# Kernel tuning notes

Hardware: AMD Instinct MI355X
Metric: run time of the kernel (lower is better)

## Reference

```python
import jax, jax.numpy as jnp
import numpy as np

N_HEADS = 32
N_KV = 8
GROUPS = 4
D_HEAD = 64
ROPE_BASE = 10000.0


def _rope_tables(seq_len):
    # inv_freq over even dims, emb = [freqs, freqs] along last axis (torch cat([outer]*2))
    inv_freq = 1.0 / (ROPE_BASE ** (jnp.arange(0, D_HEAD, 2, dtype=jnp.float32) / D_HEAD))
    t = jnp.arange(seq_len, dtype=jnp.float32)
    freqs = jnp.outer(t, inv_freq)                      # [S, D_HEAD/2]
    emb = jnp.concatenate([freqs, freqs], axis=-1)      # [S, D_HEAD]
    return jnp.cos(emb), jnp.sin(emb)


def _rotate_half(x):
    h = x.shape[-1] // 2
    return jnp.concatenate([-x[..., h:], x[..., :h]], axis=-1)


def setup_inputs() -> dict:
    key = jax.random.key(0)
    ks = jax.random.split(key, 5)
    B, S, D = 4, 2048, 2048
    s = 0.02
    return {
        "x": jax.random.normal(ks[0], (B, S, D), dtype=jnp.float32),
        "Wq": jax.random.normal(ks[1], (D, D), dtype=jnp.float32) * s,
        "Wk": jax.random.normal(ks[2], (N_KV * D_HEAD, D), dtype=jnp.float32) * s,
        "Wv": jax.random.normal(ks[3], (N_KV * D_HEAD, D), dtype=jnp.float32) * s,
        "Wo": jax.random.normal(ks[4], (D, D), dtype=jnp.float32) * s,
        "temperature": jnp.float32(1.0),
    }


def reference(x, Wq, Wk, Wv, Wo, temperature):
    B, S, D = x.shape
    # QKV projections (torch Linear: x @ W.T)
    Q = jnp.einsum('bsd,ed->bse', x, Wq).reshape(B, S, N_HEADS, D_HEAD).transpose(0, 2, 1, 3)
    K = jnp.einsum('bsd,ed->bse', x, Wk).reshape(B, S, N_KV, D_HEAD).transpose(0, 2, 1, 3)
    V = jnp.einsum('bsd,ed->bse', x, Wv).reshape(B, S, N_KV, D_HEAD).transpose(0, 2, 1, 3)

    # RoPE (offset=0, no past_kv)
    cos, sin = _rope_tables(S)          # [S, D_HEAD]
    cos = cos[None, None]
    sin = sin[None, None]
    Q = Q * cos + _rotate_half(Q) * sin
    K = K * cos + _rotate_half(K) * sin

    kv_cache = (K, V)  # pre-expansion cache, as in original

    # GQA expand: each kv head repeated GROUPS times along head axis
    Ke = jnp.repeat(K, GROUPS, axis=1)  # [B, N_HEADS, S, D_HEAD]
    Ve = jnp.repeat(V, GROUPS, axis=1)

    # scale uses .item() in torch -> constant w.r.t. autograd
    scale = (D_HEAD ** -0.5) / jnp.maximum(jnp.abs(temperature), 1e-6)
    scale = jax.lax.stop_gradient(scale)

    scores = jnp.einsum('bhqd,bhkd->bhqk', Q, Ke) * scale
    causal = jnp.tril(jnp.ones((S, S), dtype=bool))
    scores = jnp.where(causal[None, None], scores, jnp.finfo(scores.dtype).min)
    attn = jax.nn.softmax(scores, axis=-1)
    out = jnp.einsum('bhqk,bhkd->bhqd', attn, Ve)       # [B, H, S, D_HEAD]

    out = out.transpose(0, 2, 1, 3).reshape(B, S, D)
    y = jnp.einsum('bsd,ed->bse', out, Wo)
    return (y, kv_cache[0], kv_cache[1])
```

## Files before the change

kernel.cpp:

```cpp
#include <hip/hip_runtime.h>

#define S_LEN  2048
#define DMODEL 2048
#define NH     32
#define NKV    8
#define DH     64

typedef _Float16 h8   __attribute__((ext_vector_type(8)));
typedef _Float16 h4   __attribute__((ext_vector_type(4)));
typedef float    f32x4 __attribute__((ext_vector_type(4)));

__device__ __forceinline__ void load_lds16(const _Float16* g, _Float16* l) {
  typedef const __attribute__((address_space(1))) unsigned int* gp_t;
  typedef __attribute__((address_space(3))) unsigned int* lp_t;
  __builtin_amdgcn_global_load_lds((gp_t)g, (lp_t)l, 16, 0, 0);
}

#define N8_X  2097152
#define N8_WQ 524288
#define N8_WK 131072
#define N8_WV 131072
#define N8_WO 524288
#define N8_ALL (N8_X + N8_WQ + N8_WK + N8_WV + N8_WO)
__global__ void cvt_all(const float* __restrict__ x, const float* __restrict__ wq,
                        const float* __restrict__ wk, const float* __restrict__ wv,
                        const float* __restrict__ wo, _Float16* __restrict__ dst) {
  int stride = gridDim.x * blockDim.x;
  for (int i = blockIdx.x * blockDim.x + threadIdx.x; i < N8_ALL; i += stride) {
    const float* s;
    int off;
    if (i < N8_X) { s = x; off = i; }
    else if (i < N8_X + N8_WQ) { s = wq; off = i - N8_X; }
    else if (i < N8_X + N8_WQ + N8_WK) { s = wk; off = i - (N8_X + N8_WQ); }
    else if (i < N8_X + N8_WQ + N8_WK + N8_WV) { s = wv; off = i - (N8_X + N8_WQ + N8_WK); }
    else { s = wo; off = i - (N8_X + N8_WQ + N8_WK + N8_WV); }
    float4 a = ((const float4*)s)[2 * off];
    float4 b = ((const float4*)s)[2 * off + 1];
    h8 v = {(_Float16)a.x, (_Float16)a.y, (_Float16)a.z, (_Float16)a.w,
            (_Float16)b.x, (_Float16)b.y, (_Float16)b.z, (_Float16)b.w};
    ((h8*)dst)[i] = v;
  }
}

__global__ void rope_table_k(float2* __restrict__ tab) {
  int i = blockIdx.x * blockDim.x + threadIdx.x;
  int s = i >> 5, d = i & 31;
  float invf = (float)exp2(-(double)d * 0.4152410118609203);
  float angf = (float)s * invf;
  double a = (double)angf;
  const double twopi = 6.283185307179586476925287;
  a -= floor(a / twopi) * twopi;
  tab[i] = make_float2((float)cos(a), (float)sin(a));
}

template <int MODE>
__global__ __launch_bounds__(256) void gemm128(
    const _Float16* __restrict__ A, const _Float16* __restrict__ Bm,
    _Float16* __restrict__ qH, _Float16* __restrict__ kH, float* __restrict__ kF,
    _Float16* __restrict__ vH, float* __restrict__ vF, float* __restrict__ yF,
    const float2* __restrict__ rtab, const float* __restrict__ tptr) {
  __shared__ __align__(16) _Float16 lA[128 * 32];
  __shared__ __align__(16) _Float16 lB[128 * 32];
  const int Kd = 2048;
  int t = threadIdx.x;
  int w = t >> 6, lane = t & 63;
  int n0 = blockIdx.x * 128, m0 = blockIdx.y * 128;
  int wr = w >> 1, wc = w & 1;
  int lq = lane & 15, hi = lane >> 4;

  const _Float16* gA = A + (size_t)(m0 + w * 32 + (lane >> 2)) * Kd + (lane & 3) * 8;
  const _Float16* gB = Bm + (size_t)(n0 + w * 32 + (lane >> 2)) * Kd + (lane & 3) * 8;
  _Float16* dA0 = &lA[(w * 32) * 32];
  _Float16* dA1 = &lA[(w * 32 + 16) * 32];
  _Float16* dB0 = &lB[(w * 32) * 32];
  _Float16* dB1 = &lB[(w * 32 + 16) * 32];

  f32x4 z4 = {0.f, 0.f, 0.f, 0.f};
  f32x4 acc[4][4];
#pragma unroll
  for (int i = 0; i < 4; i++)
#pragma unroll
    for (int j = 0; j < 4; j++) acc[i][j] = z4;

  for (int k0 = 0; k0 < Kd; k0 += 32) {
    __syncthreads();
    load_lds16(gA + k0, dA0);
    load_lds16(gA + (size_t)16 * Kd + k0, dA1);
    load_lds16(gB + k0, dB0);
    load_lds16(gB + (size_t)16 * Kd + k0, dB1);
    __syncthreads();
    h8 af[4], bf[4];
#pragma unroll
    for (int i = 0; i < 4; i++)
      af[i] = *(const h8*)&lA[(wr * 64 + i * 16 + lq) * 32 + hi * 8];
#pragma unroll
    for (int j = 0; j < 4; j++)
      bf[j] = *(const h8*)&lB[(wc * 64 + j * 16 + lq) * 32 + hi * 8];
#pragma unroll
    for (int i = 0; i < 4; i++)
#pragma unroll
      for (int j = 0; j < 4; j++)
        acc[i][j] = __builtin_amdgcn_mfma_f32_16x16x32_f16(af[i], bf[j], acc[i][j], 0, 0, 0);
  }

  if (MODE == 3) {
#pragma unroll
    for (int ci = 0; ci < 4; ci++) {
      int col = n0 + wc * 64 + ci * 16 + lq;
#pragma unroll
      for (int ri = 0; ri < 4; ri++)
#pragma unroll
        for (int r = 0; r < 4; r++) {
          int m = m0 + wr * 64 + ri * 16 + hi * 4 + r;
          yF[(size_t)m * DMODEL + col] = acc[ri][ci][r];
        }
    }
  } else {
    int base64 = n0 + wc * 64;
    if (base64 < 2048) {
      float qsc = 0.125f / fmaxf(fabsf(tptr[0]), 1e-6f) * 1.4426950408889634f;
      int head = base64 >> 6;
#pragma unroll
      for (int ci = 0; ci < 2; ci++) {
        int dlo = ci * 16 + lq;
#pragma unroll
        for (int ri = 0; ri < 4; ri++)
#pragma unroll
          for (int r = 0; r < 4; r++) {
            int m = m0 + wr * 64 + ri * 16 + hi * 4 + r;
            int b = m >> 11, s = m & 2047;
            float2 cs = rtab[s * 32 + dlo];
            float lo = acc[ri][ci][r], hv = acc[ri][ci + 2][r];
            float olo = (lo * cs.x - hv * cs.y) * qsc;
            float ohi = (hv * cs.x + lo * cs.y) * qsc;
            size_t base = ((size_t)(b * NH + head) * S_LEN + s) * DH;
            qH[base + dlo] = (_Float16)olo;
            qH[base + dlo + 32] = (_Float16)ohi;
          }
      }
    } else if (base64 < 2560) {
      int head = (base64 - 2048) >> 6;
#pragma unroll
      for (int ci = 0; ci < 2; ci++) {
        int dlo = ci * 16 + lq;
#pragma unroll
        for (int ri = 0; ri < 4; ri++)
#pragma unroll
          for (int r = 0; r < 4; r++) {
            int m = m0 + wr * 64 + ri * 16 + hi * 4 + r;
            int b = m >> 11, s = m & 2047;
            float2 cs = rtab[s * 32 + dlo];
            float lo = acc[ri][ci][r], hv = acc[ri][ci + 2][r];
            float olo = lo * cs.x - hv * cs.y;
            float ohi = hv * cs.x + lo * cs.y;
            size_t bb = ((size_t)(b * NKV + head) * S_LEN + s) * DH;
            kH[bb + dlo] = (_Float16)olo;
            kH[bb + dlo + 32] = (_Float16)ohi;
            kF[bb + dlo] = olo;
            kF[bb + dlo + 32] = ohi;
          }
      }
    } else {
      int head = (base64 - 2560) >> 6;
#pragma unroll
      for (int ci = 0; ci < 4; ci++) {
        int d = ci * 16 + lq;
#pragma unroll
        for (int ri = 0; ri < 4; ri++)
#pragma unroll
          for (int r = 0; r < 4; r++) {
            int m = m0 + wr * 64 + ri * 16 + hi * 4 + r;
            int b = m >> 11, s = m & 2047;
            float v = acc[ri][ci][r];
            vH[((size_t)(b * NKV + head) * DH + d) * S_LEN + s] = (_Float16)v;
            vF[((size_t)(b * NKV + head) * S_LEN + s) * DH + d] = v;
          }
      }
    }
  }
}

__global__ __launch_bounds__(256, 3) void attn_fwd(
    const _Float16* __restrict__ Q, const _Float16* __restrict__ K,
    const _Float16* __restrict__ Vt, _Float16* __restrict__ AO) {
  __shared__ __align__(16) _Float16 lP[4][32 * 72];
  __shared__ __align__(16) _Float16 lV[2][64 * 64];
  int t = threadIdx.x, w = t >> 6, lane = t & 63;
  int lq = lane & 15, hi = lane >> 4;

  int bh = blockIdx.x * 16 + (blockIdx.y & 15);
  int qb = 15 - (blockIdx.y >> 4);
  int b = bh >> 5, h = bh & 31, g = h >> 2;

  const _Float16* Qp = Q + ((size_t)(b * NH + h) * S_LEN) * DH;
  const _Float16* Kp = K + ((size_t)(b * NKV + g) * S_LEN) * DH;
  const _Float16* Vp = Vt + ((size_t)(b * NKV + g) * DH) * S_LEN;

  f32x4 z4 = {0.f, 0.f, 0.f, 0.f};
  int q0 = qb * 128 + w * 32;

  size_t so0 = (size_t)(w * 16 + (lane >> 3)) * S_LEN + (size_t)(((lane & 7) ^ (lane >> 3)) * 8);
  size_t so1 = so0 + (size_t)8 * S_LEN;

  h8 qf[2][2];
#pragma unroll
  for (int cf = 0; cf < 2; cf++)
#pragma unroll
    for (int dc = 0; dc < 2; dc++)
      qf[cf][dc] = *(const h8*)&Qp[(size_t)(q0 + lq + 16 * cf) * DH + dc * 32 + hi * 8];

  f32x4 ot[4][2];
#pragma unroll
  for (int rf = 0; rf < 4; rf++)
#pragma unroll
    for (int cf = 0; cf < 2; cf++) ot[rf][cf] = z4;
  float mrun[2] = {-3e38f, -3e38f};
  float lrun[2] = {0.f, 0.f};

  int NT = 2 * qb + 2;

  load_lds16(Vp + so0, &lV[0][(w * 16) * 64]);
  load_lds16(Vp + so1, &lV[0][(w * 16 + 8) * 64]);
  h8 kf[2][4];
#pragma unroll
  for (int dc = 0; dc < 2; dc++)
#pragma unroll
    for (int rf = 0; rf < 4; rf++)
      kf[dc][rf] = *(const h8*)&Kp[(size_t)(rf * 16 + lq) * DH + dc * 32 + hi * 8];

  for (int tk = 0; tk < NT; tk++) {
    int kv0 = tk * 64;

    f32x4 sc[4][2];
#pragma unroll
    for (int rf = 0; rf < 4; rf++)
#pragma unroll
      for (int cf = 0; cf < 2; cf++) sc[rf][cf] = z4;
#pragma unroll
    for (int dc = 0; dc < 2; dc++)
#pragma unroll
      for (int rf = 0; rf < 4; rf++)
#pragma unroll
        for (int cf = 0; cf < 2; cf++)
          sc[rf][cf] = __builtin_amdgcn_mfma_f32_16x16x32_f16(kf[dc][rf], qf[cf][dc], sc[rf][cf], 0, 0, 0);

    {
      int kvn = kv0 + 64;
#pragma unroll
      for (int dc = 0; dc < 2; dc++)
#pragma unroll
        for (int rf = 0; rf < 4; rf++)
          kf[dc][rf] = *(const h8*)&Kp[(size_t)(kvn + rf * 16 + lq) * DH + dc * 32 + hi * 8];
    }

    if (kv0 + 63 > q0) {
#pragma unroll
      for (int rf = 0; rf < 4; rf++)
#pragma unroll
        for (int cf = 0; cf < 2; cf++)
#pragma unroll
          for (int r = 0; r < 4; r++) {
            int kv = kv0 + rf * 16 + hi * 4 + r;
            int q = q0 + lq + 16 * cf;
            if (kv > q) sc[rf][cf][r] = -1e30f;
          }
    }

    float mt[2];
#pragma unroll
    for (int cf = 0; cf < 2; cf++) {
      float m2 = -3e38f;
#pragma unroll
      for (int rf = 0; rf < 4; rf++)
#pragma unroll
        for (int r = 0; r < 4; r++) m2 = fmaxf(m2, sc[rf][cf][r]);
      m2 = fmaxf(m2, __shfl_xor(m2, 16));
      m2 = fmaxf(m2, __shfl_xor(m2, 32));
      mt[cf] = m2;
    }

    bool need = !__all((mt[0] - mrun[0] <= 8.f) && (mt[1] - mrun[1] <= 8.f));
    if (need) {
#pragma unroll
      for (int cf = 0; cf < 2; cf++) {
        float mnew = fmaxf(mrun[cf], mt[cf]);
        float al = __builtin_amdgcn_exp2f(mrun[cf] - mnew);
        mrun[cf] = mnew;
        lrun[cf] *= al;
#pragma unroll
        for (int rf = 0; rf < 4; rf++)
#pragma unroll
          for (int r = 0; r < 4; r++) ot[rf][cf][r] *= al;
      }
    }

    float ls[2] = {0.f, 0.f};
#pragma unroll
    for (int rf = 0; rf < 4; rf++)
#pragma unroll
      for (int cf = 0; cf < 2; cf++)
#pragma unroll
        for (int r = 0; r < 4; r++) {
          float p = __builtin_amdgcn_exp2f(sc[rf][cf][r] - mrun[cf]);
          sc[rf][cf][r] = p;
          ls[cf] += p;
        }
#pragma unroll
    for (int cf = 0; cf < 2; cf++) {
      float s2 = ls[cf];
      s2 += __shfl_xor(s2, 16);
      s2 += __shfl_xor(s2, 32);
      lrun[cf] += s2;
    }

#pragma unroll
    for (int rf = 0; rf < 4; rf++)
#pragma unroll
      for (int cf = 0; cf < 2; cf++) {
        h4 p4;
#pragma unroll
        for (int r = 0; r < 4; r++) p4[r] = (_Float16)sc[rf][cf][r];
        *(h4*)&lP[w][(lq + 16 * cf) * 72 + rf * 16 + hi * 4] = p4;
      }
    asm volatile("s_waitcnt lgkmcnt(0)" ::: "memory");
    __builtin_amdgcn_sched_barrier(0);

    asm volatile("s_waitcnt vmcnt(0)" ::: "memory");
    __builtin_amdgcn_s_barrier();

    {
      _Float16* nb = &lV[(tk + 1) & 1][0];
      size_t kvn = (size_t)(kv0 + 64);
      load_lds16(Vp + so0 + kvn, nb + (w * 16) * 64);
      load_lds16(Vp + so1 + kvn, nb + (w * 16 + 8) * 64);
    }

    {
      const _Float16* vb = &lV[tk & 1][0];
#pragma unroll
      for (int kvc = 0; kvc < 2; kvc++) {
        h8 vf[4];
#pragma unroll
        for (int rf = 0; rf < 4; rf++)
          vf[rf] = *(const h8*)&vb[(rf * 16 + lq) * 64 + (((kvc * 4 + hi) ^ (lq & 7)) * 8)];
        h8 pb[2];
#pragma unroll
        for (int cf = 0; cf < 2; cf++)
          pb[cf] = *(const h8*)&lP[w][(lq + 16 * cf) * 72 + kvc * 32 + hi * 8];
#pragma unroll
        for (int rf = 0; rf < 4; rf++)
#pragma unroll
          for (int cf = 0; cf < 2; cf++)
            ot[rf][cf] = __builtin_amdgcn_mfma_f32_16x16x32_f16(vf[rf], pb[cf], ot[rf][cf], 0, 0, 0);
      }
    }

    asm volatile("s_waitcnt lgkmcnt(0)" ::: "memory");
    __builtin_amdgcn_s_barrier();
  }

#pragma unroll
  for (int cf = 0; cf < 2; cf++) {
    float inv = 1.0f / lrun[cf];
    size_t row = (size_t)b * S_LEN + q0 + lq + 16 * cf;
#pragma unroll
    for (int rf = 0; rf < 4; rf++) {
      h4 o;
#pragma unroll
      for (int r = 0; r < 4; r++) o[r] = (_Float16)(ot[rf][cf][r] * inv);
      *(h4*)&AO[row * DMODEL + h * DH + rf * 16 + hi * 4] = o;
    }
  }
}

extern "C" void kernel_launch(void* const* d_in, const int* in_sizes, int n_in,
                              void* d_out, int out_size, void* d_ws, size_t ws_size,
                              hipStream_t stream) {
  const float* x  = (const float*)d_in[0];
  const float* Wq = (const float*)d_in[1];
  const float* Wk = (const float*)d_in[2];
  const float* Wv = (const float*)d_in[3];
  const float* Wo = (const float*)d_in[4];
  const float* tp = (const float*)d_in[5];

  float* y  = (float*)d_out;
  float* Ko = y + (size_t)16777216;
  float* Vo = Ko + (size_t)4194304;

  _Float16* xh  = (_Float16*)d_ws;
  _Float16* wqh = xh + 16777216;
  _Float16* wkh = wqh + 4194304;
  _Float16* wvh = wkh + 1048576;
  _Float16* woh = wvh + 1048576;
  _Float16* Kh  = woh + 4194304;
  _Float16* Vth = Kh + 4194304;
  float2*   rtab = (float2*)(Vth + 4194304);
  _Float16* AOh = xh;
  _Float16* Qh  = (_Float16*)d_out;
  (void)wkh; (void)wvh;

  cvt_all<<<2048, 256, 0, stream>>>(x, Wq, Wk, Wv, Wo, xh);
  rope_table_k<<<256, 256, 0, stream>>>(rtab);

  gemm128<1><<<dim3(24, 64), 256, 0, stream>>>(xh, wqh, Qh, Kh, Ko, Vth, Vo, nullptr, rtab, tp);
  attn_fwd<<<dim3(8, 256), 256, 0, stream>>>(Qh, Kh, Vth, AOh);
  gemm128<3><<<dim3(16, 64), 256, 0, stream>>>(AOh, woh, nullptr, nullptr, nullptr, nullptr, nullptr, y, rtab, tp);
}
```

Baseline: 459.2 us.

## Stage K tiles through double-buffered LDS shared by all waves

Measured after the change: 404.6 us. 1.13x faster.

```diff
diff --git a/kernel.cpp b/kernel.cpp
--- a/kernel.cpp
+++ b/kernel.cpp
@@ -184,6 +184,7 @@
     const _Float16* __restrict__ Q, const _Float16* __restrict__ K,
     const _Float16* __restrict__ Vt, _Float16* __restrict__ AO) {
   __shared__ __align__(16) _Float16 lP[4][32 * 72];
+  __shared__ __align__(16) _Float16 lK[2][64 * 64];
   __shared__ __align__(16) _Float16 lV[2][64 * 64];
   int t = threadIdx.x, w = t >> 6, lane = t & 63;
   int lq = lane & 15, hi = lane >> 4;
@@ -199,8 +200,9 @@
   f32x4 z4 = {0.f, 0.f, 0.f, 0.f};
   int q0 = qb * 128 + w * 32;
 
-  size_t so0 = (size_t)(w * 16 + (lane >> 3)) * S_LEN + (size_t)(((lane & 7) ^ (lane >> 3)) * 8);
-  size_t so1 = so0 + (size_t)8 * S_LEN;
+  int swz = ((lane & 7) ^ (lane >> 3)) * 8;
+  size_t sko0 = (size_t)(w * 16 + (lane >> 3)) * DH + (size_t)swz;
+  size_t svo0 = (size_t)(w * 16 + (lane >> 3)) * S_LEN + (size_t)swz;
 
   h8 qf[2][2];
 #pragma unroll
@@ -219,38 +221,46 @@
 
   int NT = 2 * qb + 2;
 
-  load_lds16(Vp + so0, &lV[0][(w * 16) * 64]);
-  load_lds16(Vp + so1, &lV[0][(w * 16 + 8) * 64]);
-  h8 kf[2][4];
-#pragma unroll
-  for (int dc = 0; dc < 2; dc++)
-#pragma unroll
-    for (int rf = 0; rf < 4; rf++)
-      kf[dc][rf] = *(const h8*)&Kp[(size_t)(rf * 16 + lq) * DH + dc * 32 + hi * 8];
+  load_lds16(Kp + sko0, &lK[0][(w * 16) * 64]);
+  load_lds16(Kp + sko0 + (size_t)8 * DH, &lK[0][(w * 16 + 8) * 64]);
+  load_lds16(Vp + svo0, &lV[0][(w * 16) * 64]);
+  load_lds16(Vp + svo0 + (size_t)8 * S_LEN, &lV[0][(w * 16 + 8) * 64]);
 
   for (int tk = 0; tk < NT; tk++) {
     int kv0 = tk * 64;
 
+    asm volatile("s_waitcnt vmcnt(0)" ::: "memory");
+    __builtin_amdgcn_s_barrier();
+
+    if (tk + 1 < NT) {
+      _Float16* nK = &lK[(tk + 1) & 1][0];
+      _Float16* nV = &lV[(tk + 1) & 1][0];
+      size_t kvn = (size_t)(kv0 + 64);
+      load_lds16(Kp + kvn * DH + sko0, nK + (w * 16) * 64);
+      load_lds16(Kp + kvn * DH + sko0 + (size_t)8 * DH, nK + (w * 16 + 8) * 64);
+      load_lds16(Vp + svo0 + kvn, nV + (w * 16) * 64);
+      load_lds16(Vp + svo0 + kvn + (size_t)8 * S_LEN, nV + (w * 16 + 8) * 64);
+    }
+
     f32x4 sc[4][2];
 #pragma unroll
     for (int rf = 0; rf < 4; rf++)
 #pragma unroll
       for (int cf = 0; cf < 2; cf++) sc[rf][cf] = z4;
-#pragma unroll
-    for (int dc = 0; dc < 2; dc++)
-#pragma unroll
-      for (int rf = 0; rf < 4; rf++)
-#pragma unroll
-        for (int cf = 0; cf < 2; cf++)
-          sc[rf][cf] = __builtin_amdgcn_mfma_f32_16x16x32_f16(kf[dc][rf], qf[cf][dc], sc[rf][cf], 0, 0, 0);
-
     {
-      int kvn = kv0 + 64;
-#pragma unroll
-      for (int dc = 0; dc < 2; dc++)
+      const _Float16* kb = &lK[tk & 1][0];
+#pragma unroll
+      for (int dc = 0; dc < 2; dc++) {
+        h8 kf[4];
 #pragma unroll
         for (int rf = 0; rf < 4; rf++)
-          kf[dc][rf] = *(const h8*)&Kp[(size_t)(kvn + rf * 16 + lq) * DH + dc * 32 + hi * 8];
+          kf[rf] = *(const h8*)&kb[(rf * 16 + lq) * 64 + (((dc * 4 + hi) ^ (lq & 7)) * 8)];
+#pragma unroll
+        for (int rf = 0; rf < 4; rf++)
+#pragma unroll
+          for (int cf = 0; cf < 2; cf++)
+            sc[rf][cf] = __builtin_amdgcn_mfma_f32_16x16x32_f16(kf[rf], qf[cf][dc], sc[rf][cf], 0, 0, 0);
+      }
     }
 
     if (kv0 + 63 > q0) {
@@ -325,16 +335,6 @@
     asm volatile("s_waitcnt lgkmcnt(0)" ::: "memory");
     __builtin_amdgcn_sched_barrier(0);
 
-    asm volatile("s_waitcnt vmcnt(0)" ::: "memory");
-    __builtin_amdgcn_s_barrier();
-
-    {
-      _Float16* nb = &lV[(tk + 1) & 1][0];
-      size_t kvn = (size_t)(kv0 + 64);
-      load_lds16(Vp + so0 + kvn, nb + (w * 16) * 64);
-      load_lds16(Vp + so1 + kvn, nb + (w * 16 + 8) * 64);
-    }
-
     {
       const _Float16* vb = &lV[tk & 1][0];
 #pragma unroll
@@ -354,9 +354,6 @@
             ot[rf][cf] = __builtin_amdgcn_mfma_f32_16x16x32_f16(vf[rf], pb[cf], ot[rf][cf], 0, 0, 0);
       }
     }
-
-    asm volatile("s_waitcnt lgkmcnt(0)" ::: "memory");
-    __builtin_amdgcn_s_barrier();
   }
 
 #pragma unroll
```
